# Kernel optimization log

Measured on AMD Instinct MI355X. Metric: run time of the kernel, lower is better.

## Reference

```python
import jax, jax.numpy as jnp
import numpy as np

NUM_HEADS = 8
TEMPERATURE = 10000.0


def sine_embed(pos, dim):
    """Sine positional embedding of 2D offsets. pos [..., 2] -> [..., dim]."""
    half = dim // 2  # dims per coordinate
    dim_t = TEMPERATURE ** (2.0 * (jnp.arange(half) // 2).astype(jnp.float32) / half)
    s = pos[..., :, None] / dim_t  # [..., 2, half]
    emb = jnp.stack([jnp.sin(s[..., 0::2]), jnp.cos(s[..., 1::2])], axis=-1)
    emb = emb.reshape(s.shape[:-1] + (half,))  # interleaved sin/cos per coord
    return emb.reshape(pos.shape[:-1] + (dim,))


def setup_inputs() -> dict:
    key = jax.random.key(0)
    ks = jax.random.split(key, 16)
    N, H, W, C, K = 2, 40, 40, 256, 100
    h = NUM_HEADS
    sc = 1.0 / np.sqrt(C)
    return {
        "query_feature": jax.random.normal(ks[0], (N, H, W, C), jnp.float32),
        "query_position": jax.random.uniform(ks[1], (N, H, W, 2), jnp.float32),
        "key_feature": jax.random.normal(ks[2], (N, K, C), jnp.float32),
        "key_position": jax.random.uniform(ks[3], (N, K, 2), jnp.float32),
        # MultiheadAttention params (torch convention: weight [out, in])
        "in_proj_w": jax.random.normal(ks[4], (3 * C, C), jnp.float32) * sc,
        "in_proj_b": jnp.zeros((3 * C,), jnp.float32),
        "out_proj_w": jax.random.normal(ks[5], (C, C), jnp.float32) * sc,
        "out_proj_b": jnp.zeros((C,), jnp.float32),
        # PositionalEncodingSineLearned MLP: sine(C) -> C -> num_heads
        "pos_w1": jax.random.normal(ks[6], (C, C), jnp.float32) * sc,
        "pos_b1": jnp.zeros((C,), jnp.float32),
        "pos_w2": jax.random.normal(ks[7], (h, C), jnp.float32) * sc,
        "pos_b2": jnp.zeros((h,), jnp.float32),
        # cat_pos branch params
        "pos_trans_w": jax.random.normal(ks[8], (2, 2), jnp.float32),
        "embed_w": jax.random.normal(ks[9], (C, C + 2), jnp.float32) * 0.01,
        "embed_b": jnp.zeros((C,), jnp.float32),
    }


def reference(query_feature, query_position, key_feature, key_position,
              in_proj_w, in_proj_b, out_proj_w, out_proj_b,
              pos_w1, pos_b1, pos_w2, pos_b2,
              pos_trans_w, embed_w, embed_b):
    N, H, W, C = query_feature.shape
    h = NUM_HEADS
    d = C // h
    q = query_feature.reshape(N, -1, C)            # [N,Q,C]
    qp = query_position.reshape(N, -1, 2)          # [N,Q,2] (scale_terms = 1.0)
    Q = q.shape[1]
    K = key_feature.shape[1]

    # pairwise relative positions: [N,Q,K,2]
    rel_pos = key_position[:, None, :, :] - qp[:, :, None, :]

    # learned sine relative positional encoding -> per-head additive bias
    pe = sine_embed(rel_pos, C)                              # [N,Q,K,C]
    hid = jax.nn.relu(pe @ pos_w1.T + pos_b1)                # [N,Q,K,C]
    bias = (hid @ pos_w2.T + pos_b2).transpose(0, 3, 1, 2)   # [N,h,Q,K]

    # multihead attention with additive relative bias
    wq, wk, wv = jnp.split(in_proj_w, 3, axis=0)
    bq, bk, bv = jnp.split(in_proj_b, 3, axis=0)
    qh = ((q @ wq.T + bq).reshape(N, Q, h, d)) * (d ** -0.5)
    kh = (key_feature @ wk.T + bk).reshape(N, K, h, d)
    vh = (key_feature @ wv.T + bv).reshape(N, K, h, d)
    scores = jnp.einsum('nqhd,nkhd->nhqk', qh, kh) + bias
    attn = jax.nn.softmax(scores, axis=-1)                   # [N,h,Q,K]
    ctx = jnp.einsum('nhqk,nkhd->nqhd', attn, vh).reshape(N, Q, C)
    refined = ctx @ out_proj_w.T + out_proj_b                # [N,Q,C]

    # cat_pos: attention-weighted relative position aggregation
    attn_w = attn.mean(axis=1)                               # [N,Q,K]
    new_rel = jnp.einsum('nqk,nqkc->nqc', attn_w, jax.lax.stop_gradient(rel_pos))
    new_pos = new_rel @ pos_trans_w.T                        # [N,Q,2]

    feat = jax.nn.relu(q + refined)
    feat = jax.nn.relu(jnp.concatenate([feat, new_pos], axis=-1) @ embed_w.T + embed_b)
    return feat.reshape(N, H, W, C)
```

## Files before the change

kernel.cpp:

```cpp
#include <hip/hip_runtime.h>
#include <math.h>

typedef __bf16 bf16x8 __attribute__((ext_vector_type(8)));
typedef __bf16 bf16x4 __attribute__((ext_vector_type(4)));
typedef float  f32x4  __attribute__((ext_vector_type(4)));


#define WS_KH    0u
#define WS_VH    51200u
#define WS_EWP   102400u
#define WS_QHB   168960u
#define WS_BIASB 578560u
#define WS_KEB   2012160u
#define WS_W1B   2038560u
#define WS_W2PB  2071328u
#define WS_QEB   2073376u

__device__ __forceinline__ float rdlane(float v, int l) {
  return __uint_as_float(__builtin_amdgcn_readlane(__float_as_uint(v), l));
}

__device__ __forceinline__ unsigned packbf(float a, float b) {
  unsigned short ua = __builtin_bit_cast(unsigned short, (__bf16)a);
  unsigned short ub = __builtin_bit_cast(unsigned short, (__bf16)b);
  return (unsigned)ua | ((unsigned)ub << 16);
}

__global__ __launch_bounds__(256, 2) void prep_kernel(
    const float* __restrict__ qfeat, const float* __restrict__ kfeat,
    const float* __restrict__ kpos, const float* __restrict__ qpos,
    const float* __restrict__ ipw, const float* __restrict__ ipb,
    const float* __restrict__ pos_w1, const float* __restrict__ pos_w2,
    const float* __restrict__ embed_w, float* __restrict__ ws)
{
  __shared__ float x[8 * 256];
  int bid = blockIdx.x, t = threadIdx.x;

  if (bid < 50) {
    int r = bid * 4 + (t >> 6);
    int u = t & 63;
    float p0 = kpos[r * 2 + 0], p1 = kpos[r * 2 + 1];
    __bf16* keb = (__bf16*)(ws + WS_KEB);
    bf16x4 o;
#pragma unroll
    for (int j = 0; j < 4; j++) {
      int col = u * 4 + j;
      int c = col >> 7, i = (col & 127) >> 1;
      float p = c ? p1 : p0;
      float inv = exp2f((float)i * (-13.287712379549449f / 64.0f));
      float v = p * inv;
      o[j] = (__bf16)((col & 1) ? __cosf(v) : __sinf(v));
    }
    *(bf16x4*)(keb + r * 264 + u * 4) = o;
  } else if (bid < 114) {
    int idx = (bid - 50) * 1024 + t * 4;
    float4 v = *(const float4*)(pos_w1 + idx);
    bf16x4 o; o[0] = (__bf16)v.x; o[1] = (__bf16)v.y; o[2] = (__bf16)v.z; o[3] = (__bf16)v.w;
    *(bf16x4*)((__bf16*)(ws + WS_W1B) + idx) = o;
  } else if (bid == 114) {
    __bf16* w2pb = (__bf16*)(ws + WS_W2PB);
    for (int i = 0; i < 16; i++) {
      int idx = t * 16 + i;
      w2pb[idx] = (idx < 2048) ? (__bf16)pos_w2[idx] : (__bf16)0.0f;
    }
  } else if (bid < 147) {
    int r0 = (bid - 115) * 8;
    for (int rr = 0; rr < 8; rr++) {
      int r = r0 + rr;
      for (int j = t; j < 260; j += 256)
        ws[WS_EWP + r * 260 + j] = (j < 258) ? embed_w[r * 258 + j] : 0.0f;
    }
  } else if (bid < 547) {
    int r0 = (bid - 147) * 8;
    for (int i = t; i < 2048; i += 256) x[i] = qfeat[(unsigned)r0 * 256u + i];
    __syncthreads();
    float acc[8]; float bq = ipb[t];
#pragma unroll
    for (int rr = 0; rr < 8; rr++) acc[rr] = bq;
    const float* wrow = ipw + (unsigned)t * 256u;
    for (int j = 0; j < 256; j += 4) {
      float4 w4 = *(const float4*)(wrow + j);
#pragma unroll
      for (int rr = 0; rr < 8; rr++) {
        float4 x4 = *(const float4*)(x + rr * 256 + j);
        acc[rr] = fmaf(x4.x, w4.x, fmaf(x4.y, w4.y, fmaf(x4.z, w4.z, fmaf(x4.w, w4.w, acc[rr]))));
      }
    }
    __bf16* qhb = (__bf16*)(ws + WS_QHB);
#pragma unroll
    for (int rr = 0; rr < 8; rr++)
      qhb[(unsigned)(r0 + rr) * 256u + t] = (__bf16)(acc[rr] * 0.17677669529663687f);
  } else if (bid < 579) {
    int b2 = bid - 547; int n = b2 >> 4, tile = b2 & 15;
    int r0l = tile * 7; int cnt = 100 - r0l; if (cnt > 7) cnt = 7; if (cnt <= 0) return;
    int r0 = n * 100 + r0l;
    for (int i = t; i < cnt * 256; i += 256) x[i] = kfeat[(unsigned)r0 * 256u + i];
    __syncthreads();
    float ak[7], av[7]; float bk = ipb[256 + t], bv = ipb[512 + t];
#pragma unroll
    for (int rr = 0; rr < 7; rr++) { ak[rr] = bk; av[rr] = bv; }
    const float* wkr = ipw + (unsigned)(256 + t) * 256u;
    const float* wvr = ipw + (unsigned)(512 + t) * 256u;
    for (int j = 0; j < 256; j += 4) {
      float4 wk4 = *(const float4*)(wkr + j);
      float4 wv4 = *(const float4*)(wvr + j);
#pragma unroll
      for (int rr = 0; rr < 7; rr++) {
        float4 x4 = *(const float4*)(x + rr * 256 + j);
        ak[rr] = fmaf(x4.x, wk4.x, fmaf(x4.y, wk4.y, fmaf(x4.z, wk4.z, fmaf(x4.w, wk4.w, ak[rr]))));
        av[rr] = fmaf(x4.x, wv4.x, fmaf(x4.y, wv4.y, fmaf(x4.z, wv4.z, fmaf(x4.w, wv4.w, av[rr]))));
      }
    }
    for (int rr = 0; rr < 7; rr++) {
      if (rr < cnt) {
        ws[WS_KH + (unsigned)(r0 + rr) * 256u + t] = ak[rr];
        ws[WS_VH + (unsigned)(r0 + rr) * 256u + t] = av[rr];
      }
    }
  } else {
    int r = (bid - 579) * 4 + (t >> 6);
    int u = t & 63;
    float p0 = qpos[r * 2 + 0], p1 = qpos[r * 2 + 1];
    __bf16* qeb = (__bf16*)(ws + WS_QEB);
    bf16x4 o;
#pragma unroll
    for (int j = 0; j < 4; j++) {
      int col = u * 4 + j;
      int c = col >> 7, i = (col & 127) >> 1;
      float p = c ? p1 : p0;
      float inv = exp2f((float)i * (-13.287712379549449f / 64.0f));
      float v = p * inv;
      o[j] = (__bf16)((col & 1) ? __cosf(v) : __sinf(v));
    }
    *(bf16x4*)(qeb + r * 256 + u * 4) = o;
  }
}

__global__ __launch_bounds__(256, 2) void bias_kernel(
    const float* __restrict__ pos_b1, const float* __restrict__ pos_b2,
    float* __restrict__ ws)
{
  __shared__ __align__(16) char qe_smem[32768];
  __shared__ __align__(16) __bf16 keb_s[256];

  int bid = blockIdx.x;
  int nk = bid / 25;
  int qt = bid - nk * 25;
  int n  = nk / 100;
  int k  = nk - n * 100;
  int q0 = n * 1600 + qt * 64;
  int t = threadIdx.x;
  int lane = t & 63, w = t >> 6;
  int l15 = lane & 15, quad = lane >> 4;

  const __bf16* keb = (const __bf16*)(ws + WS_KEB) + (unsigned)nk * 264u;
  const __bf16* qeb = (const __bf16*)(ws + WS_QEB);
  const __bf16* w1b = (const __bf16*)(ws + WS_W1B);
  const __bf16* w2pb = (const __bf16*)(ws + WS_W2PB);
  __bf16* biasb = (__bf16*)(ws + WS_BIASB);

  if (t < 32) *(bf16x8*)(keb_s + t * 8) = *(const bf16x8*)(keb + t * 8);

  {
    int r = t >> 2, sub = t & 3;
    const __bf16* src = qeb + (unsigned)(q0 + r) * 256u + sub * 64;
    char* dst = qe_smem + r * 512;
    int swz = (r & 7) << 4;
#pragma unroll
    for (int u = 0; u < 8; u++) {
      bf16x8 v = *(const bf16x8*)(src + u * 8);
      int cb = sub * 128 + u * 16;
      *(bf16x8*)(dst + (cb ^ swz)) = v;
    }
  }

  int xm = (l15 & 7) << 4;
  int colx[8];
#pragma unroll
  for (int kc = 0; kc < 8; kc++) colx[kc] = ((kc * 64 + quad * 16) ^ xm);
  const __bf16* w1p = w1b + (unsigned)(w * 64 + l15) * 256u + quad * 8;

  f32x4 zero4; zero4[0] = 0.f; zero4[1] = 0.f; zero4[2] = 0.f; zero4[3] = 0.f;

  auto rotk = [&](bf16x8 w8, bf16x8 ke) {
    bf16x8 a;
#pragma unroll
    for (int p2 = 0; p2 < 4; p2++) {
      float we = (float)w8[2 * p2], wo = (float)w8[2 * p2 + 1];
      float sk = (float)ke[2 * p2], ck = (float)ke[2 * p2 + 1];
      a[2 * p2]     = (__bf16)fmaf(wo, sk, -(we * ck));
      a[2 * p2 + 1] = (__bf16)fmaf(we, sk, wo * ck);
    }
    return a;
  };

  f32x4 acc[4][4];
#pragma unroll
  for (int ct = 0; ct < 4; ct++)
#pragma unroll
    for (int nt = 0; nt < 4; nt++) acc[ct][nt] = zero4;

  bf16x8 wc[4];
#pragma unroll
  for (int ct = 0; ct < 4; ct++) wc[ct] = *(const bf16x8*)(w1p + ct * 4096);

  __syncthreads();

#pragma unroll
  for (int kc = 0; kc < 8; kc++) {
    bf16x8 wn[4];
    int kcn = (kc + 1) & 7;
#pragma unroll
    for (int ct = 0; ct < 4; ct++)
      wn[ct] = *(const bf16x8*)(w1p + ct * 4096 + kcn * 32);

    bf16x8 ke8 = *(const bf16x8*)(keb_s + kc * 32 + quad * 8);
    bf16x8 af0 = rotk(wc[0], ke8);
    bf16x8 af1 = rotk(wc[1], ke8);
    bf16x8 af2 = rotk(wc[2], ke8);
    bf16x8 af3 = rotk(wc[3], ke8);

#pragma unroll
    for (int nt = 0; nt < 4; nt++) {
      bf16x8 qf = *(const bf16x8*)(qe_smem + (nt * 16 + l15) * 512 + colx[kc]);
      acc[0][nt] = __builtin_amdgcn_mfma_f32_16x16x32_bf16(af0, qf, acc[0][nt], 0, 0, 0);
      acc[1][nt] = __builtin_amdgcn_mfma_f32_16x16x32_bf16(af1, qf, acc[1][nt], 0, 0, 0);
      acc[2][nt] = __builtin_amdgcn_mfma_f32_16x16x32_bf16(af2, qf, acc[2][nt], 0, 0, 0);
      acc[3][nt] = __builtin_amdgcn_mfma_f32_16x16x32_bf16(af3, qf, acc[3][nt], 0, 0, 0);
    }
#pragma unroll
    for (int ct = 0; ct < 4; ct++) wc[ct] = wn[ct];
  }

  float b1a[4][4];
#pragma unroll
  for (int ct = 0; ct < 4; ct++)
#pragma unroll
    for (int r = 0; r < 4; r++) b1a[ct][r] = pos_b1[w * 64 + ct * 16 + quad * 4 + r];
  bf16x8 w2f[8];
#pragma unroll
  for (int kc = 0; kc < 8; kc++)
    w2f[kc] = *(const bf16x8*)(w2pb + (unsigned)l15 * 256u + kc * 32 + quad * 8);

  __syncthreads();

#pragma unroll
  for (int ct = 0; ct < 4; ct++) {
#pragma unroll
    for (int nt = 0; nt < 4; nt++) {
      int q = nt * 16 + l15;
      unsigned lo = packbf(fmaxf(acc[ct][nt][0] + b1a[ct][0], 0.f),
                           fmaxf(acc[ct][nt][1] + b1a[ct][1], 0.f));
      unsigned hi = packbf(fmaxf(acc[ct][nt][2] + b1a[ct][2], 0.f),
                           fmaxf(acc[ct][nt][3] + b1a[ct][3], 0.f));
      int cbyte = w * 128 + ct * 32 + quad * 8;
      char* p = qe_smem + q * 512 + (cbyte ^ ((q & 7) << 4));
      unsigned long long v = (unsigned long long)lo | ((unsigned long long)hi << 32);
      *(unsigned long long*)p = v;
    }
  }
  __syncthreads();

  {
    int row = w * 16 + l15;
    const char* hbase = qe_smem + row * 512;
    int hxm = (l15 & 7) << 4;
    f32x4 acc2 = zero4;
#pragma unroll
    for (int kc = 0; kc < 8; kc++) {
      bf16x8 hf = *(const bf16x8*)(hbase + ((kc * 64 + quad * 16) ^ hxm));
      acc2 = __builtin_amdgcn_mfma_f32_16x16x32_bf16(w2f[kc], hf, acc2, 0, 0, 0);
    }
    if (quad < 2) {
      int qg = q0 + row;
      bf16x4 o;
#pragma unroll
      for (int r = 0; r < 4; r++) o[r] = (__bf16)(acc2[r] + pos_b2[quad * 4 + r]);
      *(bf16x4*)(biasb + (unsigned)qg * 896u + (unsigned)k * 8u + quad * 4) = o;
    }
  }
}

__global__ __launch_bounds__(256, 4) void attn_kernel(
    const float* __restrict__ qfeat, const float* __restrict__ qpos,
    const float* __restrict__ kpos,
    const float* __restrict__ out_w, const float* __restrict__ out_b,
    const float* __restrict__ embed_b, const float* __restrict__ ptw,
    const float* __restrict__ ws, float* __restrict__ out)
{
  __shared__ float qh_s[4 * 8 * 36];
  __shared__ float attn_s[4 * 8 * 116];
  __shared__ float ctx_s[4 * 264];
  __shared__ float cat_s[4 * 264];
  __shared__ float aw_s[4 * 104];

  int bid = blockIdx.x;
  int qg0 = bid * 4;
  int n = bid / 400;
  int t = threadIdx.x;

  const __bf16* qhb = (const __bf16*)(ws + WS_QHB);
  const __bf16* biasb = (const __bf16*)(ws + WS_BIASB);
  const float* kh = ws + WS_KH;
  const float* vh = ws + WS_VH;
  const float* ewp = ws + WS_EWP;

  for (int i = t; i < 1024; i += 256) {
    int q = i >> 8, c = i & 255;
    qh_s[(q * 8 + (c >> 5)) * 36 + (c & 31)] = (float)qhb[(unsigned)(qg0 + q) * 256u + c];
  }
  __syncthreads();

  for (int i = 0; i < 4; i++) {
    int p = t + i * 256;
    if (p < 800) {
      int k = p >> 3, h = p & 7;
      const float4* kf = (const float4*)(kh + (unsigned)(n * 100 + k) * 256u + h * 32);
      float4 kv[8];
#pragma unroll
      for (int dd = 0; dd < 8; dd++) kv[dd] = kf[dd];
#pragma unroll
      for (int q = 0; q < 4; q++) {
        const float4* qf = (const float4*)(qh_s + (q * 8 + h) * 36);
        float s = (float)biasb[((unsigned)(qg0 + q) * 112u + k) * 8u + h];
#pragma unroll
        for (int dd = 0; dd < 8; dd++) {
          float4 qv = qf[dd];
          s += kv[dd].x * qv.x + kv[dd].y * qv.y + kv[dd].z * qv.z + kv[dd].w * qv.w;
        }
        attn_s[(q * 8 + h) * 116 + k] = s;
      }
    }
  }
  __syncthreads();

  {
    int q = t >> 6, h = (t >> 3) & 7, j = t & 7;
    float* row = attn_s + (q * 8 + h) * 116;
    float mx = -1e30f;
    for (int k = j; k < 100; k += 8) mx = fmaxf(mx, row[k]);
    mx = fmaxf(mx, __shfl_xor(mx, 1, 8));
    mx = fmaxf(mx, __shfl_xor(mx, 2, 8));
    mx = fmaxf(mx, __shfl_xor(mx, 4, 8));
    float sum = 0.f;
    for (int k = j; k < 100; k += 8) { float e = __expf(row[k] - mx); row[k] = e; sum += e; }
    sum += __shfl_xor(sum, 1, 8);
    sum += __shfl_xor(sum, 2, 8);
    sum += __shfl_xor(sum, 4, 8);
    float inv = 1.0f / sum;
    for (int k = j; k < 100; k += 8) row[k] *= inv;
  }
  __syncthreads();

  for (int p = t; p < 416; p += 256) {
    int q = p / 104, k = p % 104;
    if (k < 100) {
      float s = 0.f;
#pragma unroll
      for (int h = 0; h < 8; h++) s += attn_s[(q * 8 + h) * 116 + k];
      aw_s[q * 104 + k] = s * 0.125f;
    }
  }
  {
    int c = t, h = c >> 5;
    float a0 = 0.f, a1 = 0.f, a2 = 0.f, a3 = 0.f;
    const float* vp = vh + (unsigned)(n * 100) * 256u + c;
    const float* r0 = attn_s + (0 * 8 + h) * 116;
    const float* r1 = attn_s + (1 * 8 + h) * 116;
    const float* r2 = attn_s + (2 * 8 + h) * 116;
    const float* r3 = attn_s + (3 * 8 + h) * 116;
#pragma unroll 4
    for (int k = 0; k < 100; k++) {
      float vv = vp[(unsigned)k * 256u];
      a0 = fmaf(r0[k], vv, a0);
      a1 = fmaf(r1[k], vv, a1);
      a2 = fmaf(r2[k], vv, a2);
      a3 = fmaf(r3[k], vv, a3);
    }
    ctx_s[0 * 264 + c] = a0; ctx_s[1 * 264 + c] = a1;
    ctx_s[2 * 264 + c] = a2; ctx_s[3 * 264 + c] = a3;
  }
  __syncthreads();

  if (t < 8) {
    int q = t >> 1, cd = t & 1;
    float qp = qpos[(qg0 + q) * 2 + cd];
    float s = 0.f;
    for (int k = 0; k < 100; k++)
      s = fmaf(aw_s[q * 104 + k], kpos[(n * 100 + k) * 2 + cd] - qp, s);
    float so = __shfl_xor(s, 1, 2);
    if (cd == 0) cat_s[q * 264 + 256] = ptw[0] * s + ptw[1] * so;
    else         cat_s[q * 264 + 257] = ptw[2] * so + ptw[3] * s;
  }

  {
    int c = t, lane = t & 63;
    float ob = out_b[c];
    float acc0 = ob, acc1 = ob, acc2 = ob, acc3 = ob;
    const float* wr = out_w + (unsigned)c * 256u;
    for (int ch = 0; ch < 4; ch++) {
      float v0 = ctx_s[0 * 264 + ch * 64 + lane];
      float v1 = ctx_s[1 * 264 + ch * 64 + lane];
      float v2 = ctx_s[2 * 264 + ch * 64 + lane];
      float v3 = ctx_s[3 * 264 + ch * 64 + lane];
      const float* wp = wr + ch * 64;
#pragma unroll 4
      for (int j4 = 0; j4 < 16; j4++) {
        float4 w4 = *(const float4*)(wp + j4 * 4);
        int jb = j4 * 4;
        acc0 = fmaf(rdlane(v0, jb + 0), w4.x, acc0);
        acc1 = fmaf(rdlane(v1, jb + 0), w4.x, acc1);
        acc2 = fmaf(rdlane(v2, jb + 0), w4.x, acc2);
        acc3 = fmaf(rdlane(v3, jb + 0), w4.x, acc3);
        acc0 = fmaf(rdlane(v0, jb + 1), w4.y, acc0);
        acc1 = fmaf(rdlane(v1, jb + 1), w4.y, acc1);
        acc2 = fmaf(rdlane(v2, jb + 1), w4.y, acc2);
        acc3 = fmaf(rdlane(v3, jb + 1), w4.y, acc3);
        acc0 = fmaf(rdlane(v0, jb + 2), w4.z, acc0);
        acc1 = fmaf(rdlane(v1, jb + 2), w4.z, acc1);
        acc2 = fmaf(rdlane(v2, jb + 2), w4.z, acc2);
        acc3 = fmaf(rdlane(v3, jb + 2), w4.z, acc3);
        acc0 = fmaf(rdlane(v0, jb + 3), w4.w, acc0);
        acc1 = fmaf(rdlane(v1, jb + 3), w4.w, acc1);
        acc2 = fmaf(rdlane(v2, jb + 3), w4.w, acc2);
        acc3 = fmaf(rdlane(v3, jb + 3), w4.w, acc3);
      }
    }
    cat_s[0 * 264 + c] = fmaxf(qfeat[(unsigned)(qg0 + 0) * 256u + c] + acc0, 0.f);
    cat_s[1 * 264 + c] = fmaxf(qfeat[(unsigned)(qg0 + 1) * 256u + c] + acc1, 0.f);
    cat_s[2 * 264 + c] = fmaxf(qfeat[(unsigned)(qg0 + 2) * 256u + c] + acc2, 0.f);
    cat_s[3 * 264 + c] = fmaxf(qfeat[(unsigned)(qg0 + 3) * 256u + c] + acc3, 0.f);
  }
  __syncthreads();

  {
    int c = t, lane = t & 63;
    float eb = embed_b[c];
    float acc0 = eb, acc1 = eb, acc2 = eb, acc3 = eb;
    const float* er = ewp + (unsigned)c * 260u;
    for (int ch = 0; ch < 4; ch++) {
      float v0 = cat_s[0 * 264 + ch * 64 + lane];
      float v1 = cat_s[1 * 264 + ch * 64 + lane];
      float v2 = cat_s[2 * 264 + ch * 64 + lane];
      float v3 = cat_s[3 * 264 + ch * 64 + lane];
      const float* wp = er + ch * 64;
#pragma unroll 4
      for (int j4 = 0; j4 < 16; j4++) {
        float4 w4 = *(const float4*)(wp + j4 * 4);
        int jb = j4 * 4;
        acc0 = fmaf(rdlane(v0, jb + 0), w4.x, acc0);
        acc1 = fmaf(rdlane(v1, jb + 0), w4.x, acc1);
        acc2 = fmaf(rdlane(v2, jb + 0), w4.x, acc2);
        acc3 = fmaf(rdlane(v3, jb + 0), w4.x, acc3);
        acc0 = fmaf(rdlane(v0, jb + 1), w4.y, acc0);
        acc1 = fmaf(rdlane(v1, jb + 1), w4.y, acc1);
        acc2 = fmaf(rdlane(v2, jb + 1), w4.y, acc2);
        acc3 = fmaf(rdlane(v3, jb + 1), w4.y, acc3);
        acc0 = fmaf(rdlane(v0, jb + 2), w4.z, acc0);
        acc1 = fmaf(rdlane(v1, jb + 2), w4.z, acc1);
        acc2 = fmaf(rdlane(v2, jb + 2), w4.z, acc2);
        acc3 = fmaf(rdlane(v3, jb + 2), w4.z, acc3);
        acc0 = fmaf(rdlane(v0, jb + 3), w4.w, acc0);
        acc1 = fmaf(rdlane(v1, jb + 3), w4.w, acc1);
        acc2 = fmaf(rdlane(v2, jb + 3), w4.w, acc2);
        acc3 = fmaf(rdlane(v3, jb + 3), w4.w, acc3);
      }
    }
    float4 wt = *(const float4*)(er + 256);
    acc0 += cat_s[0 * 264 + 256] * wt.x + cat_s[0 * 264 + 257] * wt.y;
    acc1 += cat_s[1 * 264 + 256] * wt.x + cat_s[1 * 264 + 257] * wt.y;
    acc2 += cat_s[2 * 264 + 256] * wt.x + cat_s[2 * 264 + 257] * wt.y;
    acc3 += cat_s[3 * 264 + 256] * wt.x + cat_s[3 * 264 + 257] * wt.y;
    out[(unsigned)(qg0 + 0) * 256u + c] = fmaxf(acc0, 0.f);
    out[(unsigned)(qg0 + 1) * 256u + c] = fmaxf(acc1, 0.f);
    out[(unsigned)(qg0 + 2) * 256u + c] = fmaxf(acc2, 0.f);
    out[(unsigned)(qg0 + 3) * 256u + c] = fmaxf(acc3, 0.f);
  }
}

extern "C" void kernel_launch(void* const* d_in, const int* in_sizes, int n_in,
                              void* d_out, int out_size, void* d_ws, size_t ws_size,
                              hipStream_t stream)
{
  const float* query_feature  = (const float*)d_in[0];
  const float* query_position = (const float*)d_in[1];
  const float* key_feature    = (const float*)d_in[2];
  const float* key_position   = (const float*)d_in[3];
  const float* in_proj_w      = (const float*)d_in[4];
  const float* in_proj_b      = (const float*)d_in[5];
  const float* out_proj_w     = (const float*)d_in[6];
  const float* out_proj_b     = (const float*)d_in[7];
  const float* pos_w1         = (const float*)d_in[8];
  const float* pos_b1         = (const float*)d_in[9];
  const float* pos_w2         = (const float*)d_in[10];
  const float* pos_b2         = (const float*)d_in[11];
  const float* pos_trans_w    = (const float*)d_in[12];
  const float* embed_w        = (const float*)d_in[13];
  const float* embed_b        = (const float*)d_in[14];
  float* ws  = (float*)d_ws;
  float* out = (float*)d_out;

  hipLaunchKernelGGL(prep_kernel, dim3(1379), dim3(256), 0, stream,
                     query_feature, key_feature, key_position, query_position,
                     in_proj_w, in_proj_b, pos_w1, pos_w2, embed_w, ws);
  hipLaunchKernelGGL(bias_kernel, dim3(5000), dim3(256), 0, stream,
                     pos_b1, pos_b2, ws);
  hipLaunchKernelGGL(attn_kernel, dim3(800), dim3(256), 0, stream,
                     query_feature, query_position, key_position,
                     out_proj_w, out_proj_b, embed_b, pos_trans_w,
                     ws, out);
}
```

Measured before the change: 300.1 us.

## Reuse rotated W1 fragments across five query tiles per bias block

Each bias_kernel block now handles five 64-query tiles for one (n,k) instead of one. The key-rotated W1 fragments (af) are computed once into registers and reused for all five tiles, removing redundant global W1 loads and rotation arithmetic. A separate hidden-state LDS buffer lets the next tile's query embedding be loaded while the second MFMA stage runs. The cost is higher register pressure from 32 bf16x8 fragments, double the LDS, and only 1000 blocks, which may reduce occupancy.

After: 296.5 us. Within noise of the previous version (-1.2%).

```diff
diff --git a/kernel.cpp b/kernel.cpp
--- a/kernel.cpp
+++ b/kernel.cpp
@@ -141,14 +141,13 @@
     float* __restrict__ ws)
 {
   __shared__ __align__(16) char qe_smem[32768];
+  __shared__ __align__(16) char hid_smem[32768];
   __shared__ __align__(16) __bf16 keb_s[256];
 
   int bid = blockIdx.x;
-  int nk = bid / 25;
-  int qt = bid - nk * 25;
-  int n  = nk / 100;
-  int k  = nk - n * 100;
-  int q0 = n * 1600 + qt * 64;
+  int nk = bid / 5, g = bid - nk * 5;
+  int n = nk / 100, k = nk - n * 100;
+  int qbase = n * 1600 + g * 320;
   int t = threadIdx.x;
   int lane = t & 63, w = t >> 6;
   int l15 = lane & 15, quad = lane >> 4;
@@ -161,16 +160,14 @@
 
   if (t < 32) *(bf16x8*)(keb_s + t * 8) = *(const bf16x8*)(keb + t * 8);
 
+  int sr = t >> 2, ssub = t & 3, sswz = (sr & 7) << 4;
   {
-    int r = t >> 2, sub = t & 3;
-    const __bf16* src = qeb + (unsigned)(q0 + r) * 256u + sub * 64;
-    char* dst = qe_smem + r * 512;
-    int swz = (r & 7) << 4;
+    const __bf16* src = qeb + (unsigned)(qbase + sr) * 256u + ssub * 64;
+    char* dst = qe_smem + sr * 512;
 #pragma unroll
     for (int u = 0; u < 8; u++) {
       bf16x8 v = *(const bf16x8*)(src + u * 8);
-      int cb = sub * 128 + u * 16;
-      *(bf16x8*)(dst + (cb ^ swz)) = v;
+      *(bf16x8*)(dst + ((ssub * 128 + u * 16) ^ sswz)) = v;
     }
   }
 
@@ -180,103 +177,110 @@
   for (int kc = 0; kc < 8; kc++) colx[kc] = ((kc * 64 + quad * 16) ^ xm);
   const __bf16* w1p = w1b + (unsigned)(w * 64 + l15) * 256u + quad * 8;
 
+  float b1a[4][4];
+#pragma unroll
+  for (int ct = 0; ct < 4; ct++)
+#pragma unroll
+    for (int r = 0; r < 4; r++) b1a[ct][r] = pos_b1[w * 64 + ct * 16 + quad * 4 + r];
+
   f32x4 zero4; zero4[0] = 0.f; zero4[1] = 0.f; zero4[2] = 0.f; zero4[3] = 0.f;
 
-  auto rotk = [&](bf16x8 w8, bf16x8 ke) {
-    bf16x8 a;
-#pragma unroll
-    for (int p2 = 0; p2 < 4; p2++) {
-      float we = (float)w8[2 * p2], wo = (float)w8[2 * p2 + 1];
-      float sk = (float)ke[2 * p2], ck = (float)ke[2 * p2 + 1];
-      a[2 * p2]     = (__bf16)fmaf(wo, sk, -(we * ck));
-      a[2 * p2 + 1] = (__bf16)fmaf(we, sk, wo * ck);
-    }
-    return a;
-  };
-
-  f32x4 acc[4][4];
-#pragma unroll
-  for (int ct = 0; ct < 4; ct++)
-#pragma unroll
-    for (int nt = 0; nt < 4; nt++) acc[ct][nt] = zero4;
-
-  bf16x8 wc[4];
-#pragma unroll
-  for (int ct = 0; ct < 4; ct++) wc[ct] = *(const bf16x8*)(w1p + ct * 4096);
-
   __syncthreads();
 
+  bf16x8 af[8][4];
 #pragma unroll
   for (int kc = 0; kc < 8; kc++) {
-    bf16x8 wn[4];
-    int kcn = (kc + 1) & 7;
+    bf16x8 ke8 = *(const bf16x8*)(keb_s + kc * 32 + quad * 8);
+#pragma unroll
+    for (int ct = 0; ct < 4; ct++) {
+      bf16x8 w8 = *(const bf16x8*)(w1p + ct * 4096 + kc * 32);
+      bf16x8 a;
+#pragma unroll
+      for (int p2 = 0; p2 < 4; p2++) {
+        float we = (float)w8[2 * p2], wo = (float)w8[2 * p2 + 1];
+        float sk = (float)ke8[2 * p2], ck = (float)ke8[2 * p2 + 1];
+        a[2 * p2]     = (__bf16)fmaf(wo, sk, -(we * ck));
+        a[2 * p2 + 1] = (__bf16)fmaf(we, sk, wo * ck);
+      }
+      af[kc][ct] = a;
+    }
+  }
+
+#pragma unroll 1
+  for (int tt = 0; tt < 5; tt++) {
+    f32x4 acc[4][4];
 #pragma unroll
     for (int ct = 0; ct < 4; ct++)
-      wn[ct] = *(const bf16x8*)(w1p + ct * 4096 + kcn * 32);
-
-    bf16x8 ke8 = *(const bf16x8*)(keb_s + kc * 32 + quad * 8);
-    bf16x8 af0 = rotk(wc[0], ke8);
-    bf16x8 af1 = rotk(wc[1], ke8);
-    bf16x8 af2 = rotk(wc[2], ke8);
-    bf16x8 af3 = rotk(wc[3], ke8);
-
-#pragma unroll
-    for (int nt = 0; nt < 4; nt++) {
-      bf16x8 qf = *(const bf16x8*)(qe_smem + (nt * 16 + l15) * 512 + colx[kc]);
-      acc[0][nt] = __builtin_amdgcn_mfma_f32_16x16x32_bf16(af0, qf, acc[0][nt], 0, 0, 0);
-      acc[1][nt] = __builtin_amdgcn_mfma_f32_16x16x32_bf16(af1, qf, acc[1][nt], 0, 0, 0);
-      acc[2][nt] = __builtin_amdgcn_mfma_f32_16x16x32_bf16(af2, qf, acc[2][nt], 0, 0, 0);
-      acc[3][nt] = __builtin_amdgcn_mfma_f32_16x16x32_bf16(af3, qf, acc[3][nt], 0, 0, 0);
-    }
-#pragma unroll
-    for (int ct = 0; ct < 4; ct++) wc[ct] = wn[ct];
-  }
-
-  float b1a[4][4];
-#pragma unroll
-  for (int ct = 0; ct < 4; ct++)
-#pragma unroll
-    for (int r = 0; r < 4; r++) b1a[ct][r] = pos_b1[w * 64 + ct * 16 + quad * 4 + r];
-  bf16x8 w2f[8];
-#pragma unroll
-  for (int kc = 0; kc < 8; kc++)
-    w2f[kc] = *(const bf16x8*)(w2pb + (unsigned)l15 * 256u + kc * 32 + quad * 8);
-
-  __syncthreads();
-
-#pragma unroll
-  for (int ct = 0; ct < 4; ct++) {
-#pragma unroll
-    for (int nt = 0; nt < 4; nt++) {
-      int q = nt * 16 + l15;
-      unsigned lo = packbf(fmaxf(acc[ct][nt][0] + b1a[ct][0], 0.f),
-                           fmaxf(acc[ct][nt][1] + b1a[ct][1], 0.f));
-      unsigned hi = packbf(fmaxf(acc[ct][nt][2] + b1a[ct][2], 0.f),
-                           fmaxf(acc[ct][nt][3] + b1a[ct][3], 0.f));
-      int cbyte = w * 128 + ct * 32 + quad * 8;
-      char* p = qe_smem + q * 512 + (cbyte ^ ((q & 7) << 4));
-      unsigned long long v = (unsigned long long)lo | ((unsigned long long)hi << 32);
-      *(unsigned long long*)p = v;
-    }
-  }
-  __syncthreads();
-
-  {
-    int row = w * 16 + l15;
-    const char* hbase = qe_smem + row * 512;
-    int hxm = (l15 & 7) << 4;
-    f32x4 acc2 = zero4;
+#pragma unroll
+      for (int nt = 0; nt < 4; nt++) acc[ct][nt] = zero4;
+
 #pragma unroll
     for (int kc = 0; kc < 8; kc++) {
-      bf16x8 hf = *(const bf16x8*)(hbase + ((kc * 64 + quad * 16) ^ hxm));
-      acc2 = __builtin_amdgcn_mfma_f32_16x16x32_bf16(w2f[kc], hf, acc2, 0, 0, 0);
-    }
-    if (quad < 2) {
-      int qg = q0 + row;
-      bf16x4 o;
-#pragma unroll
-      for (int r = 0; r < 4; r++) o[r] = (__bf16)(acc2[r] + pos_b2[quad * 4 + r]);
-      *(bf16x4*)(biasb + (unsigned)qg * 896u + (unsigned)k * 8u + quad * 4) = o;
+#pragma unroll
+      for (int nt = 0; nt < 4; nt++) {
+        bf16x8 qf = *(const bf16x8*)(qe_smem + (nt * 16 + l15) * 512 + colx[kc]);
+        acc[0][nt] = __builtin_amdgcn_mfma_f32_16x16x32_bf16(af[kc][0], qf, acc[0][nt], 0, 0, 0);
+        acc[1][nt] = __builtin_amdgcn_mfma_f32_16x16x32_bf16(af[kc][1], qf, acc[1][nt], 0, 0, 0);
+        acc[2][nt] = __builtin_amdgcn_mfma_f32_16x16x32_bf16(af[kc][2], qf, acc[2][nt], 0, 0, 0);
+        acc[3][nt] = __builtin_amdgcn_mfma_f32_16x16x32_bf16(af[kc][3], qf, acc[3][nt], 0, 0, 0);
+      }
+    }
+
+#pragma unroll
+    for (int ct = 0; ct < 4; ct++) {
+#pragma unroll
+      for (int nt = 0; nt < 4; nt++) {
+        int q = nt * 16 + l15;
+        unsigned lo = packbf(fmaxf(acc[ct][nt][0] + b1a[ct][0], 0.f),
+                             fmaxf(acc[ct][nt][1] + b1a[ct][1], 0.f));
+        unsigned hi = packbf(fmaxf(acc[ct][nt][2] + b1a[ct][2], 0.f),
+                             fmaxf(acc[ct][nt][3] + b1a[ct][3], 0.f));
+        int cbyte = w * 128 + ct * 32 + quad * 8;
+        char* p = hid_smem + q * 512 + (cbyte ^ ((q & 7) << 4));
+        unsigned long long v = (unsigned long long)lo | ((unsigned long long)hi << 32);
+        *(unsigned long long*)p = v;
+      }
+    }
+
+    bf16x8 w2f[8];
+#pragma unroll
+    for (int kc = 0; kc < 8; kc++)
+      w2f[kc] = *(const bf16x8*)(w2pb + (unsigned)l15 * 256u + kc * 32 + quad * 8);
+
+    __syncthreads();
+
+    bf16x8 qv[8];
+    if (tt < 4) {
+      const __bf16* src = qeb + (unsigned)(qbase + (tt + 1) * 64 + sr) * 256u + ssub * 64;
+#pragma unroll
+      for (int u = 0; u < 8; u++) qv[u] = *(const bf16x8*)(src + u * 8);
+    }
+
+    {
+      int row = w * 16 + l15;
+      const char* hbase = hid_smem + row * 512;
+      int hxm = (l15 & 7) << 4;
+      f32x4 acc2 = zero4;
+#pragma unroll
+      for (int kc = 0; kc < 8; kc++) {
+        bf16x8 hf = *(const bf16x8*)(hbase + ((kc * 64 + quad * 16) ^ hxm));
+        acc2 = __builtin_amdgcn_mfma_f32_16x16x32_bf16(w2f[kc], hf, acc2, 0, 0, 0);
+      }
+      if (quad < 2) {
+        int qg = qbase + tt * 64 + row;
+        bf16x4 o;
+#pragma unroll
+        for (int r = 0; r < 4; r++) o[r] = (__bf16)(acc2[r] + pos_b2[quad * 4 + r]);
+        *(bf16x4*)(biasb + (unsigned)qg * 896u + (unsigned)k * 8u + quad * 4) = o;
+      }
+    }
+
+    if (tt < 4) {
+      char* dst = qe_smem + sr * 512;
+#pragma unroll
+      for (int u = 0; u < 8; u++)
+        *(bf16x8*)(dst + ((ssub * 128 + u * 16) ^ sswz)) = qv[u];
+      __syncthreads();
     }
   }
 }
@@ -503,7 +507,7 @@
   hipLaunchKernelGGL(prep_kernel, dim3(1379), dim3(256), 0, stream,
                      query_feature, key_feature, key_position, query_position,
                      in_proj_w, in_proj_b, pos_w1, pos_w2, embed_w, ws);
-  hipLaunchKernelGGL(bias_kernel, dim3(5000), dim3(256), 0, stream,
+  hipLaunchKernelGGL(bias_kernel, dim3(1000), dim3(256), 0, stream,
                      pos_b1, pos_b2, ws);
   hipLaunchKernelGGL(attn_kernel, dim3(800), dim3(256), 0, stream,
                      query_feature, query_position, key_position,
```
